# Performance work log

Hardware: AMD Instinct MI355X
Metric: run time of the kernel (lower is better)

Reference implementation:

```python
import jax, jax.numpy as jnp
import numpy as np

N, D, H, E, C = 10000, 256, 512, 320000, 1  # nodes, feature_dim, nhid, edges, nclass


def setup_inputs() -> dict:
    key = jax.random.key(0)
    ks = jax.random.split(key, 8)
    x = jax.random.normal(ks[0], (N, D), jnp.float32)
    edge_src = jax.random.randint(ks[1], (E,), 0, N, jnp.int32)
    edge_dst = jax.random.randint(ks[2], (E,), 0, N, jnp.int32)
    # adjacency values of a row-normalized A (mean aggregation); ~1/avg_degree scale
    edge_val = jax.random.uniform(ks[3], (E,), jnp.float32) / 32.0
    W_conv = jax.random.normal(ks[4], (2 * D, H), jnp.float32) / np.sqrt(2 * D)
    b_conv = jnp.zeros((H,), jnp.float32)
    W1 = jax.random.normal(ks[5], (H, H), jnp.float32) / np.sqrt(H)
    b1 = jnp.zeros((H,), jnp.float32)
    prelu_a = jnp.full((H,), 0.25, jnp.float32)  # PReLU per-channel slope (torch init 0.25)
    W2 = jax.random.normal(ks[6], (H, C), jnp.float32) / np.sqrt(H)
    b2 = jnp.zeros((C,), jnp.float32)
    return dict(x=x, edge_src=edge_src, edge_dst=edge_dst, edge_val=edge_val,
                W_conv=W_conv, b_conv=b_conv, W1=W1, b1=b1,
                prelu_a=prelu_a, W2=W2, b2=b2)


def reference(x, edge_src, edge_dst, edge_val, W_conv, b_conv, W1, b1, prelu_a, W2, b2):
    # MeanAggregator: agg = spmm(A, x) with A given as (dst, src, val) edge list
    msgs = x[edge_src] * edge_val[:, None]                         # [E, D] gather + scale
    agg = jax.ops.segment_sum(msgs, edge_dst, num_segments=x.shape[0])  # [N, D]
    # GraphConv: concat(self, agg) -> linear -> ReLU
    cat = jnp.concatenate([x, agg], axis=-1)                       # [N, 2D]
    h = jax.nn.relu(cat @ W_conv + b_conv)                         # [N, H]
    # classifier: Linear -> PReLU -> Linear, then view(-1)
    z = h @ W1 + b1                                                # [N, H]
    z = jnp.where(z > 0, z, prelu_a * z)                           # PReLU(nhid)
    pred = (z @ W2 + b2).reshape(-1)                               # [N * nclass]
    return pred
```

## Files before the change

### kernel.cpp

```cpp
#include <hip/hip_runtime.h>
#include <hip/hip_bf16.h>

#define N_NODES 10000
#define M_PAD   10112
#define DIM     256
#define HID     512
#define KDIM    512
#define N_EDGE  320000
#define ELL_W   128

typedef __attribute__((ext_vector_type(4))) float  f32x4;
typedef __attribute__((ext_vector_type(8))) __bf16 bf16x8;

__device__ __forceinline__ unsigned short f2bf(float f) {
    union { float f; unsigned int u; } v; v.f = f;
    unsigned int r = v.u + 0x7FFFu + ((v.u >> 16) & 1u);
    return (unsigned short)(r >> 16);
}
__device__ __forceinline__ float bf2f(unsigned short u) {
    union { unsigned int i; float f; } v; v.i = ((unsigned int)u) << 16;
    return v.f;
}

__global__ void k_zero(int* __restrict__ deg) {
    int i = blockIdx.x * 256 + threadIdx.x;
    if (i < 10240) deg[i] = 0;
}

__device__ __forceinline__ void wtrans(const float* __restrict__ W,
                                       unsigned short* __restrict__ Wt,
                                       int tb, float (*tile)[65]) {
    const int t  = threadIdx.x;
    const int kb = (tb >> 3) * 64, nb = (tb & 7) * 64;
    const int r    = t >> 2;
    const int cseg = (t & 3) * 16;
    const float* src = W + (size_t)(kb + r) * 512 + nb + cseg;
    #pragma unroll
    for (int j = 0; j < 4; ++j)
        *(f32x4*)&tile[r][cseg + 4 * j] = *(const f32x4*)(src + 4 * j);
    __syncthreads();
    unsigned short* dst = Wt + (size_t)(nb + r) * 512 + kb + cseg;
    #pragma unroll
    for (int j = 0; j < 4; ++j) {
        ushort4 o;
        o.x = f2bf(tile[cseg + 4 * j + 0][r]);
        o.y = f2bf(tile[cseg + 4 * j + 1][r]);
        o.z = f2bf(tile[cseg + 4 * j + 2][r]);
        o.w = f2bf(tile[cseg + 4 * j + 3][r]);
        *(ushort4*)(dst + 4 * j) = o;
    }
}

__global__ void k_prep(const int* __restrict__ esrc, const int* __restrict__ edst,
                       const float* __restrict__ eval,
                       int* __restrict__ deg, int2* __restrict__ ell,
                       const float* __restrict__ x, unsigned short* __restrict__ cat,
                       const float* __restrict__ Wc, unsigned short* __restrict__ Wct,
                       const float* __restrict__ W1, unsigned short* __restrict__ W1t) {
    __shared__ float tile[64][65];
    int b = blockIdx.x;
    if (b < 1250) {
        int e = b * 256 + threadIdx.x;
        if (e < N_EDGE) {
            int d = edst[e];
            int slot = atomicAdd(&deg[d], 1);
            if (slot < ELL_W)
                ell[(size_t)d * ELL_W + slot] = make_int2(esrc[e], __float_as_int(eval[e]));
        }
    } else if (b < 3750) {
        int t  = (b - 1250) * 256 + threadIdx.x;
        int n  = t >> 6;
        int c4 = (t & 63) * 4;
        f32x4 v = *(const f32x4*)(x + (size_t)n * DIM + c4);
        ushort4 o;
        o.x = f2bf(v.x); o.y = f2bf(v.y); o.z = f2bf(v.z); o.w = f2bf(v.w);
        *(ushort4*)(cat + (size_t)n * 2 * DIM + c4) = o;
    } else if (b < 3814) {
        wtrans(Wc, Wct, b - 3750, tile);
    } else {
        wtrans(W1, W1t, b - 3814, tile);
    }
}

__global__ void k_agg(const int* __restrict__ deg, const int2* __restrict__ ell,
                      unsigned short* __restrict__ cat) {
    int wid  = (blockIdx.x * blockDim.x + threadIdx.x) >> 6;
    int lane = threadIdx.x & 63;
    if (wid >= N_NODES) return;
    int cnt = deg[wid];
    if (cnt > ELL_W) cnt = ELL_W;
    const int2* row = ell + (size_t)wid * ELL_W;
    int c4 = lane * 4;
    f32x4 a0 = {0.f,0.f,0.f,0.f}, a1 = a0, a2 = a0, a3 = a0;
    f32x4 a4 = a0, a5 = a0, a6 = a0, a7 = a0;
    for (int base = 0; base < cnt; base += 64) {
        int m = cnt - base;
        if (m > 64) m = 64;
        int2 my = make_int2(0, 0);
        if (lane < m) my = row[base + lane];
        int j = 0;
        for (; j + 8 <= m; j += 8) {
            int   s0 = __builtin_amdgcn_readlane(my.x, j);
            float v0 = __int_as_float(__builtin_amdgcn_readlane(my.y, j));
            int   s1 = __builtin_amdgcn_readlane(my.x, j + 1);
            float v1 = __int_as_float(__builtin_amdgcn_readlane(my.y, j + 1));
            int   s2 = __builtin_amdgcn_readlane(my.x, j + 2);
            float v2 = __int_as_float(__builtin_amdgcn_readlane(my.y, j + 2));
            int   s3 = __builtin_amdgcn_readlane(my.x, j + 3);
            float v3 = __int_as_float(__builtin_amdgcn_readlane(my.y, j + 3));
            int   s4 = __builtin_amdgcn_readlane(my.x, j + 4);
            float v4 = __int_as_float(__builtin_amdgcn_readlane(my.y, j + 4));
            int   s5 = __builtin_amdgcn_readlane(my.x, j + 5);
            float v5 = __int_as_float(__builtin_amdgcn_readlane(my.y, j + 5));
            int   s6 = __builtin_amdgcn_readlane(my.x, j + 6);
            float v6 = __int_as_float(__builtin_amdgcn_readlane(my.y, j + 6));
            int   s7 = __builtin_amdgcn_readlane(my.x, j + 7);
            float v7 = __int_as_float(__builtin_amdgcn_readlane(my.y, j + 7));
            ushort4 q0 = *(const ushort4*)(cat + (size_t)s0 * 2 * DIM + c4);
            ushort4 q1 = *(const ushort4*)(cat + (size_t)s1 * 2 * DIM + c4);
            ushort4 q2 = *(const ushort4*)(cat + (size_t)s2 * 2 * DIM + c4);
            ushort4 q3 = *(const ushort4*)(cat + (size_t)s3 * 2 * DIM + c4);
            ushort4 q4 = *(const ushort4*)(cat + (size_t)s4 * 2 * DIM + c4);
            ushort4 q5 = *(const ushort4*)(cat + (size_t)s5 * 2 * DIM + c4);
            ushort4 q6 = *(const ushort4*)(cat + (size_t)s6 * 2 * DIM + c4);
            ushort4 q7 = *(const ushort4*)(cat + (size_t)s7 * 2 * DIM + c4);
            a0.x += v0 * bf2f(q0.x); a0.y += v0 * bf2f(q0.y);
            a0.z += v0 * bf2f(q0.z); a0.w += v0 * bf2f(q0.w);
            a1.x += v1 * bf2f(q1.x); a1.y += v1 * bf2f(q1.y);
            a1.z += v1 * bf2f(q1.z); a1.w += v1 * bf2f(q1.w);
            a2.x += v2 * bf2f(q2.x); a2.y += v2 * bf2f(q2.y);
            a2.z += v2 * bf2f(q2.z); a2.w += v2 * bf2f(q2.w);
            a3.x += v3 * bf2f(q3.x); a3.y += v3 * bf2f(q3.y);
            a3.z += v3 * bf2f(q3.z); a3.w += v3 * bf2f(q3.w);
            a4.x += v4 * bf2f(q4.x); a4.y += v4 * bf2f(q4.y);
            a4.z += v4 * bf2f(q4.z); a4.w += v4 * bf2f(q4.w);
            a5.x += v5 * bf2f(q5.x); a5.y += v5 * bf2f(q5.y);
            a5.z += v5 * bf2f(q5.z); a5.w += v5 * bf2f(q5.w);
            a6.x += v6 * bf2f(q6.x); a6.y += v6 * bf2f(q6.y);
            a6.z += v6 * bf2f(q6.z); a6.w += v6 * bf2f(q6.w);
            a7.x += v7 * bf2f(q7.x); a7.y += v7 * bf2f(q7.y);
            a7.z += v7 * bf2f(q7.z); a7.w += v7 * bf2f(q7.w);
        }
        for (; j < m; ++j) {
            int   s0 = __builtin_amdgcn_readlane(my.x, j);
            float v0 = __int_as_float(__builtin_amdgcn_readlane(my.y, j));
            ushort4 q0 = *(const ushort4*)(cat + (size_t)s0 * 2 * DIM + c4);
            a0.x += v0 * bf2f(q0.x); a0.y += v0 * bf2f(q0.y);
            a0.z += v0 * bf2f(q0.z); a0.w += v0 * bf2f(q0.w);
        }
    }
    ushort4 o;
    o.x = f2bf(((a0.x + a1.x) + (a2.x + a3.x)) + ((a4.x + a5.x) + (a6.x + a7.x)));
    o.y = f2bf(((a0.y + a1.y) + (a2.y + a3.y)) + ((a4.y + a5.y) + (a6.y + a7.y)));
    o.z = f2bf(((a0.z + a1.z) + (a2.z + a3.z)) + ((a4.z + a5.z) + (a6.z + a7.z)));
    o.w = f2bf(((a0.w + a1.w) + (a2.w + a3.w)) + ((a4.w + a5.w) + (a6.w + a7.w)));
    *(ushort4*)(cat + (size_t)wid * 2 * DIM + DIM + c4) = o;
}

#define LDSW 72

#define LOAD4(dst, p) { dst[0] = *(const f32x4*)(p); dst[1] = *(const f32x4*)((p) + 8); \
                        dst[2] = *(const f32x4*)((p) + 16); dst[3] = *(const f32x4*)((p) + 24); }
#define STORE4(p, src) { *(f32x4*)(p) = src[0]; *(f32x4*)((p) + 8) = src[1]; \
                         *(f32x4*)((p) + 16) = src[2]; *(f32x4*)((p) + 24) = src[3]; }

template <int MODE>
__global__ __launch_bounds__(256)
void k_gemm128(const unsigned short* __restrict__ A,
               const unsigned short* __restrict__ Bt,
               const float* __restrict__ bias,
               const float* __restrict__ pa,
               const float* __restrict__ w2,
               unsigned short* __restrict__ hout,
               float* __restrict__ part) {
    __shared__ unsigned short As[2][128 * LDSW];
    __shared__ unsigned short Bs[2][128 * LDSW];

    const int t    = threadIdx.x;
    const int lane = t & 63;
    const int w    = t >> 6;
    const int wr   = w >> 1, wc = w & 1;
    const int tn   = blockIdx.x & 3;
    const int tm   = blockIdx.x >> 2;
    const int gm0  = tm * 128, gn0 = tn * 128;

    const int srow = t >> 1;
    const int scol = (t & 1) * 32;
    const unsigned short* gA = A  + (size_t)(gm0 + srow) * KDIM + scol;
    const unsigned short* gB = Bt + (size_t)(gn0 + srow) * KDIM + scol;
    const int woff = srow * LDSW + scol;

    const int r15 = lane & 15;
    const int kf  = (lane >> 4) * 8;

    f32x4 acc[4][4] = {};
    f32x4 va[4], vb[4];

    LOAD4(va, gA);
    LOAD4(vb, gB);
    STORE4(&As[0][woff], va);
    STORE4(&Bs[0][woff], vb);
    __syncthreads();

    #pragma unroll
    for (int ks = 0; ks < 8; ++ks) {
        const int cur = ks & 1;
        if (ks < 7) {
            gA += 64; gB += 64;
            LOAD4(va, gA);
            LOAD4(vb, gB);
        }
        #pragma unroll
        for (int kk = 0; kk < 2; ++kk) {
            bf16x8 af[4], bf[4];
            #pragma unroll
            for (int m = 0; m < 4; ++m)
                af[m] = *(const bf16x8*)&As[cur][(wr * 64 + m * 16 + r15) * LDSW + kk * 32 + kf];
            #pragma unroll
            for (int n = 0; n < 4; ++n)
                bf[n] = *(const bf16x8*)&Bs[cur][(wc * 64 + n * 16 + r15) * LDSW + kk * 32 + kf];
            #pragma unroll
            for (int m = 0; m < 4; ++m)
                #pragma unroll
                for (int n = 0; n < 4; ++n)
                    acc[m][n] = __builtin_amdgcn_mfma_f32_16x16x32_bf16(af[m], bf[n], acc[m][n], 0, 0, 0);
        }
        if (ks < 7) {
            STORE4(&As[cur ^ 1][woff], va);
            STORE4(&Bs[cur ^ 1][woff], vb);
            __syncthreads();
        }
    }

    const int rq = lane >> 4;
    if (MODE == 0) {
        #pragma unroll
        for (int n = 0; n < 4; ++n) {
            int c = gn0 + wc * 64 + n * 16 + r15;
            float b = bias[c];
            #pragma unroll
            for (int m = 0; m < 4; ++m) {
                #pragma unroll
                for (int i = 0; i < 4; ++i) {
                    int row = gm0 + wr * 64 + m * 16 + rq * 4 + i;
                    float v = acc[m][n][i] + b;
                    v = v > 0.f ? v : 0.f;
                    hout[(size_t)row * HID + c] = f2bf(v);
                }
            }
        }
    } else {
        float rsum[4][4] = {};
        #pragma unroll
        for (int n = 0; n < 4; ++n) {
            int c = gn0 + wc * 64 + n * 16 + r15;
            float b = bias[c];
            float a = pa[c];
            float wv = w2[c];
            #pragma unroll
            for (int m = 0; m < 4; ++m)
                #pragma unroll
                for (int i = 0; i < 4; ++i) {
                    float v = acc[m][n][i] + b;
                    v = v > 0.f ? v : a * v;
                    rsum[m][i] += v * wv;
                }
        }
        #pragma unroll
        for (int m = 0; m < 4; ++m)
            #pragma unroll
            for (int i = 0; i < 4; ++i) {
                float s = rsum[m][i];
                s += __shfl_xor(s, 1);
                s += __shfl_xor(s, 2);
                s += __shfl_xor(s, 4);
                s += __shfl_xor(s, 8);
                if (r15 == 0) {
                    int row = gm0 + wr * 64 + m * 16 + rq * 4 + i;
                    part[(size_t)(tn * 2 + wc) * M_PAD + row] = s;
                }
            }
    }
}

__global__ void k_vout(const float* __restrict__ part, const float* __restrict__ b2,
                       float* __restrict__ pred) {
    int row = blockIdx.x * blockDim.x + threadIdx.x;
    if (row >= N_NODES) return;
    float s = b2[0];
    #pragma unroll
    for (int j = 0; j < 8; ++j) s += part[(size_t)j * M_PAD + row];
    pred[row] = s;
}

extern "C" void kernel_launch(void* const* d_in, const int* in_sizes, int n_in,
                              void* d_out, int out_size, void* d_ws, size_t ws_size,
                              hipStream_t stream) {
    const float* x    = (const float*)d_in[0];
    const int*   esrc = (const int*)  d_in[1];
    const int*   edst = (const int*)  d_in[2];
    const float* eval = (const float*)d_in[3];
    const float* Wc   = (const float*)d_in[4];
    const float* bc   = (const float*)d_in[5];
    const float* W1   = (const float*)d_in[6];
    const float* b1   = (const float*)d_in[7];
    const float* pa   = (const float*)d_in[8];
    const float* W2   = (const float*)d_in[9];
    const float* b2   = (const float*)d_in[10];
    float* pred = (float*)d_out;

    char* w = (char*)d_ws;
    int*            deg   = (int*)w;
    int2*           ell   = (int2*)(w + 40960);
    unsigned short* cat   = (unsigned short*)(w + 10526720);
    unsigned short* Wct   = (unsigned short*)(w + 20881408);
    unsigned short* W1t   = (unsigned short*)(w + 21405696);
    unsigned short* h     = (unsigned short*)(w + 21929984);
    float*          partb = (float*)(w + 32284672);

    k_zero<<<40, 256, 0, stream>>>(deg);

    k_prep<<<3878, 256, 0, stream>>>(esrc, edst, eval, deg, ell, x, cat, Wc, Wct, W1, W1t);

    k_agg<<<(N_NODES * 64 + 255) / 256, 256, 0, stream>>>(deg, ell, cat);

    k_gemm128<0><<<316, 256, 0, stream>>>(cat, Wct, bc, nullptr, nullptr, h, nullptr);
    k_gemm128<1><<<316, 256, 0, stream>>>(h, W1t, b1, pa, W2, nullptr, partb);

    k_vout<<<(N_NODES + 255) / 256, 256, 0, stream>>>(partb, b2, pred);
}
```

Baseline: 88.69 us.

## Stage GEMM tiles via direct global-to-LDS loads with XOR-swizzled layout

Replaces the register round-trip (global load to VGPRs, then LDS store) in the bf16 MFMA GEMM with global_load_lds 16-byte direct transfers into shared memory. The padded LDS layout is replaced by an unpadded 64-wide layout with an XOR swizzle on 16-byte chunks to avoid bank conflicts on the fragment reads. This is meant to cut VGPR pressure and LDS store instructions and to let the next tile's loads overlap with compute. The risk is that the single barrier per step may not ensure the async LDS writes have completed, and the swizzle indexing must match exactly.

```diff
diff --git a/kernel.cpp b/kernel.cpp
--- a/kernel.cpp
+++ b/kernel.cpp
@@ -20,6 +20,12 @@
 __device__ __forceinline__ float bf2f(unsigned short u) {
     union { unsigned int i; float f; } v; v.i = ((unsigned int)u) << 16;
     return v.f;
+}
+
+__device__ __forceinline__ void gload16(const void* g, void* l) {
+    __builtin_amdgcn_global_load_lds(
+        (const __attribute__((address_space(1))) void*)g,
+        (__attribute__((address_space(3))) void*)l, 16, 0, 0);
 }
 
 __global__ void k_zero(int* __restrict__ deg) {
@@ -157,12 +163,12 @@
     *(ushort4*)(cat + (size_t)wid * 2 * DIM + DIM + c4) = o;
 }
 
-#define LDSW 72
-
-#define LOAD4(dst, p) { dst[0] = *(const f32x4*)(p); dst[1] = *(const f32x4*)((p) + 8); \
-                        dst[2] = *(const f32x4*)((p) + 16); dst[3] = *(const f32x4*)((p) + 24); }
-#define STORE4(p, src) { *(f32x4*)(p) = src[0]; *(f32x4*)((p) + 8) = src[1]; \
-                         *(f32x4*)((p) + 16) = src[2]; *(f32x4*)((p) + 24) = src[3]; }
+#define STAGE(buf, kt) { \
+    _Pragma("unroll") \
+    for (int i = 0; i < 4; ++i) { \
+        gload16(pA + (size_t)i * 8 * KDIM + (kt) * 64, &As[buf][ldsbase + i * 512]); \
+        gload16(pB + (size_t)i * 8 * KDIM + (kt) * 64, &Bs[buf][ldsbase + i * 512]); \
+    } }
 
 template <int MODE>
 __global__ __launch_bounds__(256)
@@ -173,8 +179,8 @@
                const float* __restrict__ w2,
                unsigned short* __restrict__ hout,
                float* __restrict__ part) {
-    __shared__ unsigned short As[2][128 * LDSW];
-    __shared__ unsigned short Bs[2][128 * LDSW];
+    __shared__ unsigned short As[2][128 * 64];
+    __shared__ unsigned short Bs[2][128 * 64];
 
     const int t    = threadIdx.x;
     const int lane = t & 63;
@@ -184,52 +190,42 @@
     const int tm   = blockIdx.x >> 2;
     const int gm0  = tm * 128, gn0 = tn * 128;
 
-    const int srow = t >> 1;
-    const int scol = (t & 1) * 32;
-    const unsigned short* gA = A  + (size_t)(gm0 + srow) * KDIM + scol;
-    const unsigned short* gB = Bt + (size_t)(gn0 + srow) * KDIM + scol;
-    const int woff = srow * LDSW + scol;
+    const int srow = w * 32 + (lane >> 3);
+    const int lc   = (lane & 7) ^ (lane >> 3);
+    const unsigned short* pA = A  + (size_t)(gm0 + srow) * KDIM + lc * 8;
+    const unsigned short* pB = Bt + (size_t)(gn0 + srow) * KDIM + lc * 8;
+    const int ldsbase = w * 2048;
 
     const int r15 = lane & 15;
-    const int kf  = (lane >> 4) * 8;
+    const int hi  = lane >> 4;
+    const int x7  = r15 & 7;
 
     f32x4 acc[4][4] = {};
-    f32x4 va[4], vb[4];
-
-    LOAD4(va, gA);
-    LOAD4(vb, gB);
-    STORE4(&As[0][woff], va);
-    STORE4(&Bs[0][woff], vb);
+
+    STAGE(0, 0);
     __syncthreads();
 
     #pragma unroll
     for (int ks = 0; ks < 8; ++ks) {
         const int cur = ks & 1;
-        if (ks < 7) {
-            gA += 64; gB += 64;
-            LOAD4(va, gA);
-            LOAD4(vb, gB);
-        }
+        if (ks < 7) STAGE(cur ^ 1, ks + 1);
         #pragma unroll
         for (int kk = 0; kk < 2; ++kk) {
+            const int pc = ((kk * 4 + hi) ^ x7) * 8;
             bf16x8 af[4], bf[4];
             #pragma unroll
             for (int m = 0; m < 4; ++m)
-                af[m] = *(const bf16x8*)&As[cur][(wr * 64 + m * 16 + r15) * LDSW + kk * 32 + kf];
+                af[m] = *(const bf16x8*)&As[cur][(wr * 64 + m * 16 + r15) * 64 + pc];
             #pragma unroll
             for (int n = 0; n < 4; ++n)
-                bf[n] = *(const bf16x8*)&Bs[cur][(wc * 64 + n * 16 + r15) * LDSW + kk * 32 + kf];
+                bf[n] = *(const bf16x8*)&Bs[cur][(wc * 64 + n * 16 + r15) * 64 + pc];
             #pragma unroll
             for (int m = 0; m < 4; ++m)
                 #pragma unroll
                 for (int n = 0; n < 4; ++n)
                     acc[m][n] = __builtin_amdgcn_mfma_f32_16x16x32_bf16(af[m], bf[n], acc[m][n], 0, 0, 0);
         }
-        if (ks < 7) {
-            STORE4(&As[cur ^ 1][woff], va);
-            STORE4(&Bs[cur ^ 1][woff], vb);
-            __syncthreads();
-        }
+        if (ks < 7) __syncthreads();
     }
 
     const int rq = lane >> 4;
```

After: 88.10 us. Within noise of the previous version (-0.7%).
